# Kernel optimization log

Hardware: AMD Instinct MI355X
Metric: run time of the kernel (lower is better)

The kernel has to match this reference:

```python
import jax, jax.numpy as jnp
import numpy as np

RWKV_K_CLAMP = 60.0
B, T, C = 8, 1024, 1024
LAYER_ID, N_LAYER = 2, 12


def _decay_speed():
    # replicate RWKV_TimeMix.__init__ decay_speed construction
    first = 1
    f1 = 3.0 + (LAYER_ID - first) / (N_LAYER - 1 - first) * (1.2 - 3.0)
    f2 = 0.65 + (LAYER_ID - first) / (N_LAYER - 1 - first) * (0.4 - 0.65)
    if LAYER_ID == first:
        f1 += 0.5
    if LAYER_ID == N_LAYER - 2:
        f2 = 0.4
    if LAYER_ID == N_LAYER - 1:
        f2 = 0.37
    h = np.arange(C, dtype=np.float64)
    return (f2 ** (h / (C - 1) * 7.0)) * f1


def setup_inputs() -> dict:
    key = jax.random.key(0)
    ks = jax.random.split(key, 6)
    scale = 1.0 / np.sqrt(C)
    time_mix = np.ones((C,), np.float32)
    time_mix[: C // 2] = 0.0
    return {
        "x": jax.random.normal(ks[0], (B, T, C), jnp.float32),
        "time_decay": jnp.asarray(np.log(_decay_speed()), jnp.float32),  # (C,)
        "time_first": jnp.full((C,), np.log(0.3), jnp.float32),
        "time_mix": jnp.asarray(time_mix),
        "combined_mix": jnp.full((C,), 0.01, jnp.float32),
        "Wk": jax.random.normal(ks[1], (C, C), jnp.float32) * scale,
        "Wv": jax.random.normal(ks[2], (C, C), jnp.float32) * scale,
        "Wr": jax.random.normal(ks[3], (C, C), jnp.float32) * scale,
        "Wo": jax.random.normal(ks[4], (C, C), jnp.float32) * scale,
    }


def _wkv(w, u, k, v):
    # w,u: (C,); k,v: (B,T,C). Numerically-stable decayed linear recurrence
    # (RWKV wkv kernel: running-max, like online softmax).
    b = k.shape[0]
    init = (
        jnp.zeros((b, C), k.dtype),            # numerator state a
        jnp.zeros((b, C), k.dtype),            # denominator state b
        jnp.full((b, C), -1e38, k.dtype),      # running max exponent p
    )

    def step(carry, kv):
        a, bb, p = carry
        kt, vt = kv  # (B,C)
        no = jnp.maximum(p, u + kt)
        e1 = jnp.exp(p - no)
        e2 = jnp.exp(u + kt - no)
        y = (e1 * a + e2 * vt) / (e1 * bb + e2)
        no2 = jnp.maximum(w + p, kt)
        e1 = jnp.exp(w + p - no2)
        e2 = jnp.exp(kt - no2)
        return (e1 * a + e2 * vt, e1 * bb + e2, no2), y

    _, y = jax.lax.scan(step, init, (k.transpose(1, 0, 2), v.transpose(1, 0, 2)))
    return y.transpose(1, 0, 2)  # (B,T,C)


def reference(x, time_decay, time_first, time_mix, combined_mix, Wk, Wv, Wr, Wo):
    b, t, c = x.shape
    zrow = jnp.zeros((b, 1, c), x.dtype)
    x_m1 = jnp.concatenate([zrow, x[:, :-1, :]], axis=1)   # time_shift / x_{t-1}
    x_p1 = jnp.concatenate([x[:, 1:, :], zrow], axis=1)    # x_{t+1}
    half = c // 2
    x_comb = jnp.concatenate([x_m1[:, :, :half], x_p1[:, :, half:]], axis=-1)
    xm = x * time_mix + x_m1 * (1.0 - time_mix) + x_comb * combined_mix
    k = jnp.exp(jnp.minimum(jnp.einsum("btc,dc->btd", xm, Wk), RWKV_K_CLAMP))
    v = jnp.einsum("btc,dc->btd", xm, Wv)
    r = jnp.einsum("btc,dc->btd", xm, Wr)
    wkv = _wkv(time_decay / t, time_first / t, k, v)
    return jnp.einsum("btc,dc->btd", jax.nn.sigmoid(r) * wkv, Wo)
```

## Files before the change

kernel.cpp:

```cpp
#include <hip/hip_runtime.h>
#include <hip/hip_bf16.h>
#include <stdint.h>

#define B_SZ 8
#define T_LEN 1024
#define C_DIM 1024
#define M_ROWS (B_SZ * T_LEN)
#define NCH 32
#define CHL (T_LEN / NCH)

typedef unsigned short ushort_t;
typedef __attribute__((ext_vector_type(8))) short short8;
typedef __attribute__((ext_vector_type(4))) float f32x4;
typedef __attribute__((ext_vector_type(4))) unsigned short us4;

static __device__ __forceinline__ float bf2f(ushort_t u) {
  union { unsigned int i; float f; } x; x.i = ((unsigned int)u) << 16; return x.f;
}
static __device__ __forceinline__ ushort_t f2bf(float f) {
  union { float f; unsigned int i; } x; x.f = f;
  unsigned int r = x.i + 0x7fffu + ((x.i >> 16) & 1u);
  return (ushort_t)(r >> 16);
}

static __device__ __forceinline__ void gload_lds16(const void* g, void* l) {
  __builtin_amdgcn_global_load_lds(
      (const __attribute__((address_space(1))) void*)g,
      (__attribute__((address_space(3))) void*)l, 16, 0, 0);
}

__global__ void cvt_w_kernel(const float* __restrict__ wk, const float* __restrict__ wv,
                             const float* __restrict__ wr, const float* __restrict__ wo,
                             ushort_t* __restrict__ out) {
  int gid = blockIdx.x * 256 + threadIdx.x;
  int which = gid >> 18;
  int off = (gid << 2) & ((1 << 20) - 1);
  const float* src = which == 0 ? wk : which == 1 ? wv : which == 2 ? wr : wo;
  float4 v = *(const float4*)(src + off);
  us4 o = {f2bf(v.x), f2bf(v.y), f2bf(v.z), f2bf(v.w)};
  *(us4*)(out + (size_t)gid * 4) = o;
}

__global__ void xm_kernel(const float* __restrict__ x, const float* __restrict__ tm,
                          const float* __restrict__ cm, ushort_t* __restrict__ xmb) {
  int gid = blockIdx.x * 256 + threadIdx.x;
  int c4 = (gid & (C_DIM / 4 - 1)) * 4;
  int t = (gid >> 8) & (T_LEN - 1);
  const float4 zero = {0.f, 0.f, 0.f, 0.f};
  float4 xv = *(const float4*)(x + (size_t)gid * 4);
  float4 xp = (t > 0) ? *(const float4*)(x + (size_t)gid * 4 - C_DIM) : zero;
  float4 xn = (t < T_LEN - 1) ? *(const float4*)(x + (size_t)gid * 4 + C_DIM) : zero;
  float4 tmv = *(const float4*)(tm + c4);
  float4 cmv = *(const float4*)(cm + c4);
  float4 xc = (c4 < C_DIM / 2) ? xp : xn;
  us4 o;
  o.x = f2bf(xv.x * tmv.x + xp.x * (1.f - tmv.x) + xc.x * cmv.x);
  o.y = f2bf(xv.y * tmv.y + xp.y * (1.f - tmv.y) + xc.y * cmv.y);
  o.z = f2bf(xv.z * tmv.z + xp.z * (1.f - tmv.z) + xc.z * cmv.z);
  o.w = f2bf(xv.w * tmv.w + xp.w * (1.f - tmv.w) + xc.w * cmv.w);
  *(us4*)(xmb + (size_t)gid * 4) = o;
}

template <int FUSED>
__global__ __launch_bounds__(256) void gemm_bt(const ushort_t* __restrict__ A,
                                               const ushort_t* __restrict__ Bw,
                                               float* __restrict__ outF,
                                               ushort_t* __restrict__ outV,
                                               ushort_t* __restrict__ outR) {
  constexpr int K = 1024;
  constexpr int NT = K / 32;
  __shared__ ushort_t As[2][128 * 32];
  __shared__ ushort_t Bs[2][128 * 32];

  const int tid = threadIdx.x;
  const int lane = tid & 63;
  const int wave = tid >> 6;

  const int bid = blockIdx.x;
  const int xcd = bid & 7;
  const int r = bid >> 3;
  const int bm = (xcd * 8 + (r & 7)) * 128;
  const int jb = r >> 3;
  const int mode = FUSED ? (jb >> 3) : 3;
  const int bn = FUSED ? (jb & 7) * 128 : jb * 128;
  const ushort_t* Bp = FUSED ? (Bw + ((size_t)(jb >> 3) << 20)) : Bw;

  const int wr = (wave >> 1) * 64;
  const int wc = (wave & 1) * 64;

  f32x4 acc[4][4];
#pragma unroll
  for (int m = 0; m < 4; ++m)
#pragma unroll
    for (int n = 0; n < 4; ++n) acc[m][n] = (f32x4){0.f, 0.f, 0.f, 0.f};

  const int srow = tid >> 2;
  const int scol = (((tid & 3) ^ ((srow >> 1) & 3)) * 8);
  const ushort_t* Ag = A + (size_t)(bm + srow) * K + scol;
  const ushort_t* Bg = Bp + (size_t)(bn + srow) * K + scol;
  ushort_t* AsP0 = &As[0][tid * 8];
  ushort_t* BsP0 = &Bs[0][tid * 8];
  ushort_t* AsP1 = &As[1][tid * 8];
  ushort_t* BsP1 = &Bs[1][tid * 8];

  const int fr = lane & 15;
  const int kq = lane >> 4;
  const int ps = (kq ^ ((fr >> 1) & 3)) * 8;

  auto stage = [&](int buf, int k0) {
    ushort_t* ap = buf ? AsP1 : AsP0;
    ushort_t* bp = buf ? BsP1 : BsP0;
    gload_lds16(Ag + k0, ap);
    gload_lds16(Ag + (size_t)64 * K + k0, ap + 64 * 32);
    gload_lds16(Bg + k0, bp);
    gload_lds16(Bg + (size_t)64 * K + k0, bp + 64 * 32);
  };

  stage(0, 0);
  asm volatile("s_waitcnt vmcnt(0)" ::: "memory");
  __syncthreads();

  int cur = 0;
  for (int t = 0; t < NT; ++t) {
    if (t < NT - 1) stage(cur ^ 1, (t + 1) * 32);
    short8 af[4], bfr[4];
#pragma unroll
    for (int m = 0; m < 4; ++m)
      af[m] = *(const short8*)&As[cur][(wr + m * 16 + fr) * 32 + ps];
#pragma unroll
    for (int n = 0; n < 4; ++n)
      bfr[n] = *(const short8*)&Bs[cur][(wc + n * 16 + fr) * 32 + ps];
#pragma unroll
    for (int m = 0; m < 4; ++m)
#pragma unroll
      for (int n = 0; n < 4; ++n)
        acc[m][n] = __builtin_amdgcn_mfma_f32_16x16x32_bf16(af[m], bfr[n], acc[m][n], 0, 0, 0);
    asm volatile("s_waitcnt vmcnt(0)" ::: "memory");
    __syncthreads();
    cur ^= 1;
  }

  const int crow0 = (lane >> 4) * 4;
#pragma unroll
  for (int m = 0; m < 4; ++m)
#pragma unroll
    for (int n = 0; n < 4; ++n)
#pragma unroll
      for (int j = 0; j < 4; ++j) {
        float v = acc[m][n][j];
        size_t idx = (size_t)(bm + wr + m * 16 + crow0 + j) * C_DIM + (bn + wc + n * 16 + fr);
        if (mode == 0) {
          outF[idx] = __expf(fminf(v, 60.f));
        } else if (mode == 1) {
          outV[idx] = f2bf(v);
        } else if (mode == 2) {
          outR[idx] = f2bf(1.f / (1.f + __expf(-v)));
        } else {
          outF[idx] = v;
        }
      }
}

__global__ void wkv_phaseA(const float* __restrict__ kk, const ushort_t* __restrict__ vv,
                           const float* __restrict__ td,
                           float* __restrict__ sa, float* __restrict__ sb,
                           float* __restrict__ sp) {
  int gid = blockIdx.x * 256 + threadIdx.x;
  int c = gid & (C_DIM - 1);
  int ch = (gid >> 10) & (NCH - 1);
  int b = gid >> 15;
  float w = td[c] * (1.f / T_LEN);
  size_t base = ((size_t)b * T_LEN + ch * CHL) * C_DIM + c;
  float a = 0.f, bb = 0.f, p = -1e38f;
  for (int t = 0; t < CHL; ++t) {
    float kt = kk[base + (size_t)t * C_DIM];
    float vt = bf2f(vv[base + (size_t)t * C_DIM]);
    float no2 = fmaxf(w + p, kt);
    float e1 = __expf(w + p - no2);
    float e2 = __expf(kt - no2);
    a = e1 * a + e2 * vt;
    bb = e1 * bb + e2;
    p = no2;
  }
  sa[gid] = a; sb[gid] = bb; sp[gid] = p;
}

__global__ void wkv_phaseC2(const float* __restrict__ kk, const ushort_t* __restrict__ vv,
                            const ushort_t* __restrict__ sr, const float* __restrict__ td,
                            const float* __restrict__ tf,
                            const float* __restrict__ sa, const float* __restrict__ sb,
                            const float* __restrict__ sp, ushort_t* __restrict__ sy) {
  int gid = blockIdx.x * 256 + threadIdx.x;
  int c = gid & (C_DIM - 1);
  int ch = (gid >> 10) & (NCH - 1);
  int b = gid >> 15;
  float w = td[c] * (1.f / T_LEN);
  float u = tf[c] * (1.f / T_LEN);
  float wL = w * (float)CHL;

  float a = 0.f, bb = 0.f, p = -1e38f;
  size_t sbase = ((size_t)b * NCH) * C_DIM + c;
  for (int j = 0; j < ch; ++j) {
    float ac = sa[sbase + (size_t)j * C_DIM];
    float bc = sb[sbase + (size_t)j * C_DIM];
    float pc = sp[sbase + (size_t)j * C_DIM];
    float pn = fmaxf(p + wL, pc);
    float e1 = __expf(p + wL - pn);
    float e2 = __expf(pc - pn);
    a = e1 * a + e2 * ac;
    bb = e1 * bb + e2 * bc;
    p = pn;
  }

  size_t base = ((size_t)b * T_LEN + ch * CHL) * C_DIM + c;
  for (int t = 0; t < CHL; ++t) {
    float kt = kk[base + (size_t)t * C_DIM];
    float vt = bf2f(vv[base + (size_t)t * C_DIM]);
    float no = fmaxf(p, u + kt);
    float e1 = __expf(p - no);
    float e2 = __expf(u + kt - no);
    float y = (e1 * a + e2 * vt) / (e1 * bb + e2);
    float srv = bf2f(sr[base + (size_t)t * C_DIM]);
    sy[base + (size_t)t * C_DIM] = f2bf(srv * y);
    float no2 = fmaxf(w + p, kt);
    e1 = __expf(w + p - no2);
    e2 = __expf(kt - no2);
    a = e1 * a + e2 * vt;
    bb = e1 * bb + e2;
    p = no2;
  }
}

extern "C" void kernel_launch(void* const* d_in, const int* in_sizes, int n_in,
                              void* d_out, int out_size, void* d_ws, size_t ws_size,
                              hipStream_t stream) {
  const float* x  = (const float*)d_in[0];
  const float* td = (const float*)d_in[1];
  const float* tf = (const float*)d_in[2];
  const float* tm = (const float*)d_in[3];
  const float* cm = (const float*)d_in[4];
  const float* Wk = (const float*)d_in[5];
  const float* Wv = (const float*)d_in[6];
  const float* Wr = (const float*)d_in[7];
  const float* Wo = (const float*)d_in[8];

  const size_t MC = (size_t)M_ROWS * C_DIM;
  const size_t CC = (size_t)C_DIM * C_DIM;

  char* ws = (char*)d_ws;
  ushort_t* xmb = (ushort_t*)ws; ws += MC * 2;
  ushort_t* Wb  = (ushort_t*)ws; ws += 4 * CC * 2;
  float*    kk  = (float*)ws;    ws += MC * 4;
  ushort_t* vv  = (ushort_t*)ws; ws += MC * 2;
  ushort_t* sr  = (ushort_t*)ws; ws += MC * 2;
  ushort_t* sy  = (ushort_t*)ws; ws += MC * 2;
  float* sa = (float*)ws; ws += (size_t)B_SZ * NCH * C_DIM * 4;
  float* sb = (float*)ws; ws += (size_t)B_SZ * NCH * C_DIM * 4;
  float* sp = (float*)ws; ws += (size_t)B_SZ * NCH * C_DIM * 4;

  cvt_w_kernel<<<(4 * CC / 4) / 256, 256, 0, stream>>>(Wk, Wv, Wr, Wo, Wb);
  xm_kernel<<<(MC / 4) / 256, 256, 0, stream>>>(x, tm, cm, xmb);

  gemm_bt<1><<<dim3(1536), 256, 0, stream>>>(xmb, Wb, kk, vv, sr);

  wkv_phaseA<<<(B_SZ * NCH * C_DIM) / 256, 256, 0, stream>>>(kk, vv, td, sa, sb, sp);
  wkv_phaseC2<<<(B_SZ * NCH * C_DIM) / 256, 256, 0, stream>>>(kk, vv, sr, td, tf, sa, sb, sp, sy);

  gemm_bt<0><<<dim3(512), 256, 0, stream>>>(sy, Wb + 3 * CC, (float*)d_out, nullptr, nullptr);
}
```

Measured before the change: 166.0 us.

## Enlarge fused QKV GEMM tiles, deepen K-step in output GEMM, store k as bf16

The fused k/v/r GEMM moves to 256x256 tiles with 512 threads and 8 waves, giving 384 blocks. This raises operand reuse per loaded byte. The output projection GEMM gets its own kernel with a 64-wide K step and an 8-way XOR swizzle, which halves the number of barrier iterations. The exp(k) intermediate is now stored as bf16 instead of fp32 to cut memory traffic in the WKV passes, at some precision cost on values that can reach exp(60).

```diff
diff --git a/kernel.cpp b/kernel.cpp
--- a/kernel.cpp
+++ b/kernel.cpp
@@ -61,59 +61,58 @@
   *(us4*)(xmb + (size_t)gid * 4) = o;
 }
 
-template <int FUSED>
-__global__ __launch_bounds__(256) void gemm_bt(const ushort_t* __restrict__ A,
-                                               const ushort_t* __restrict__ Bw,
-                                               float* __restrict__ outF,
-                                               ushort_t* __restrict__ outV,
-                                               ushort_t* __restrict__ outR) {
+__global__ __launch_bounds__(512, 2) void gemm_fused(const ushort_t* __restrict__ A,
+                                                     const ushort_t* __restrict__ Bw,
+                                                     ushort_t* __restrict__ outK,
+                                                     ushort_t* __restrict__ outV,
+                                                     ushort_t* __restrict__ outR) {
   constexpr int K = 1024;
   constexpr int NT = K / 32;
-  __shared__ ushort_t As[2][128 * 32];
-  __shared__ ushort_t Bs[2][128 * 32];
+  __shared__ ushort_t As[2][256 * 32];
+  __shared__ ushort_t Bs[2][256 * 32];
 
   const int tid = threadIdx.x;
-  const int lane = tid & 63;
-  const int wave = tid >> 6;
+  const int l = tid & 63;
+  const int w = tid >> 6;
+  const int wm = w >> 2;
+  const int wn = w & 3;
+  const int fr = l & 15;
+  const int kq = l >> 4;
+  const int ps = (kq ^ ((fr >> 1) & 3)) * 8;
 
   const int bid = blockIdx.x;
   const int xcd = bid & 7;
-  const int r = bid >> 3;
-  const int bm = (xcd * 8 + (r & 7)) * 128;
-  const int jb = r >> 3;
-  const int mode = FUSED ? (jb >> 3) : 3;
-  const int bn = FUSED ? (jb & 7) * 128 : jb * 128;
-  const ushort_t* Bp = FUSED ? (Bw + ((size_t)(jb >> 3) << 20)) : Bw;
-
-  const int wr = (wave >> 1) * 64;
-  const int wc = (wave & 1) * 64;
-
-  f32x4 acc[4][4];
-#pragma unroll
-  for (int m = 0; m < 4; ++m)
+  const int idx = bid >> 3;
+  const int jb = idx >> 2;
+  const int bm = (xcd * 4 + (idx & 3)) * 256;
+  const int mode = jb >> 2;
+  const int bn = (jb & 3) * 256;
+  const ushort_t* Bp = Bw + ((size_t)mode << 20);
+
+  f32x4 acc[8][4];
+#pragma unroll
+  for (int m = 0; m < 8; ++m)
 #pragma unroll
     for (int n = 0; n < 4; ++n) acc[m][n] = (f32x4){0.f, 0.f, 0.f, 0.f};
 
-  const int srow = tid >> 2;
-  const int scol = (((tid & 3) ^ ((srow >> 1) & 3)) * 8);
-  const ushort_t* Ag = A + (size_t)(bm + srow) * K + scol;
-  const ushort_t* Bg = Bp + (size_t)(bn + srow) * K + scol;
-  ushort_t* AsP0 = &As[0][tid * 8];
-  ushort_t* BsP0 = &Bs[0][tid * 8];
-  ushort_t* AsP1 = &As[1][tid * 8];
-  ushort_t* BsP1 = &Bs[1][tid * 8];
-
-  const int fr = lane & 15;
-  const int kq = lane >> 4;
-  const int ps = (kq ^ ((fr >> 1) & 3)) * 8;
+  int srow[2], scol[2];
+#pragma unroll
+  for (int i = 0; i < 2; ++i) {
+    int row = w * 32 + i * 16 + (l >> 2);
+    srow[i] = row;
+    scol[i] = ((l & 3) ^ ((row >> 1) & 3)) * 8;
+  }
+  const ushort_t* AgB = A + (size_t)bm * K;
+  const ushort_t* BgB = Bp + (size_t)bn * K;
+  const int dst0 = w * 1024 + l * 8;
 
   auto stage = [&](int buf, int k0) {
-    ushort_t* ap = buf ? AsP1 : AsP0;
-    ushort_t* bp = buf ? BsP1 : BsP0;
-    gload_lds16(Ag + k0, ap);
-    gload_lds16(Ag + (size_t)64 * K + k0, ap + 64 * 32);
-    gload_lds16(Bg + k0, bp);
-    gload_lds16(Bg + (size_t)64 * K + k0, bp + 64 * 32);
+#pragma unroll
+    for (int i = 0; i < 2; ++i)
+      gload_lds16(AgB + (size_t)srow[i] * K + scol[i] + k0, &As[buf][dst0 + i * 512]);
+#pragma unroll
+    for (int i = 0; i < 2; ++i)
+      gload_lds16(BgB + (size_t)srow[i] * K + scol[i] + k0, &Bs[buf][dst0 + i * 512]);
   };
 
   stage(0, 0);
@@ -123,45 +122,136 @@
   int cur = 0;
   for (int t = 0; t < NT; ++t) {
     if (t < NT - 1) stage(cur ^ 1, (t + 1) * 32);
-    short8 af[4], bfr[4];
-#pragma unroll
-    for (int m = 0; m < 4; ++m)
-      af[m] = *(const short8*)&As[cur][(wr + m * 16 + fr) * 32 + ps];
-#pragma unroll
-    for (int n = 0; n < 4; ++n)
-      bfr[n] = *(const short8*)&Bs[cur][(wc + n * 16 + fr) * 32 + ps];
-#pragma unroll
-    for (int m = 0; m < 4; ++m)
-#pragma unroll
-      for (int n = 0; n < 4; ++n)
-        acc[m][n] = __builtin_amdgcn_mfma_f32_16x16x32_bf16(af[m], bfr[n], acc[m][n], 0, 0, 0);
+    short8 af[8], bfr[4];
+#pragma unroll
+    for (int mf = 0; mf < 8; ++mf)
+      af[mf] = *(const short8*)&As[cur][(wm * 128 + mf * 16 + fr) * 32 + ps];
+#pragma unroll
+    for (int nf = 0; nf < 4; ++nf)
+      bfr[nf] = *(const short8*)&Bs[cur][(wn * 64 + nf * 16 + fr) * 32 + ps];
+#pragma unroll
+    for (int mf = 0; mf < 8; ++mf)
+#pragma unroll
+      for (int nf = 0; nf < 4; ++nf)
+        acc[mf][nf] = __builtin_amdgcn_mfma_f32_16x16x32_bf16(af[mf], bfr[nf], acc[mf][nf], 0, 0, 0);
     asm volatile("s_waitcnt vmcnt(0)" ::: "memory");
     __syncthreads();
     cur ^= 1;
   }
 
-  const int crow0 = (lane >> 4) * 4;
-#pragma unroll
-  for (int m = 0; m < 4; ++m)
-#pragma unroll
-    for (int n = 0; n < 4; ++n)
+#pragma unroll
+  for (int mf = 0; mf < 8; ++mf)
+#pragma unroll
+    for (int nf = 0; nf < 4; ++nf)
 #pragma unroll
       for (int j = 0; j < 4; ++j) {
-        float v = acc[m][n][j];
-        size_t idx = (size_t)(bm + wr + m * 16 + crow0 + j) * C_DIM + (bn + wc + n * 16 + fr);
+        float v = acc[mf][nf][j];
+        size_t ridx = (size_t)(bm + wm * 128 + mf * 16 + kq * 4 + j) * C_DIM +
+                      (bn + wn * 64 + nf * 16 + fr);
         if (mode == 0) {
-          outF[idx] = __expf(fminf(v, 60.f));
+          outK[ridx] = f2bf(__expf(fminf(v, 60.f)));
         } else if (mode == 1) {
-          outV[idx] = f2bf(v);
-        } else if (mode == 2) {
-          outR[idx] = f2bf(1.f / (1.f + __expf(-v)));
+          outV[ridx] = f2bf(v);
         } else {
-          outF[idx] = v;
+          outR[ridx] = f2bf(1.f / (1.f + __expf(-v)));
         }
       }
 }
 
-__global__ void wkv_phaseA(const float* __restrict__ kk, const ushort_t* __restrict__ vv,
+__global__ __launch_bounds__(256, 2) void gemm_out(const ushort_t* __restrict__ A,
+                                                   const ushort_t* __restrict__ Bw,
+                                                   float* __restrict__ outF) {
+  constexpr int K = 1024;
+  constexpr int NT = K / 64;
+  __shared__ ushort_t As[2][128 * 64];
+  __shared__ ushort_t Bs[2][128 * 64];
+
+  const int tid = threadIdx.x;
+  const int l = tid & 63;
+  const int wave = tid >> 6;
+  const int fr = l & 15;
+  const int kq = l >> 4;
+
+  const int bid = blockIdx.x;
+  const int xcd = bid & 7;
+  const int idx = bid >> 3;
+  const int jb = idx >> 3;
+  const int bm = (xcd * 8 + (idx & 7)) * 128;
+  const int bn = jb * 128;
+
+  const int wr = (wave >> 1) * 64;
+  const int wc = (wave & 1) * 64;
+
+  f32x4 acc[4][4];
+#pragma unroll
+  for (int m = 0; m < 4; ++m)
+#pragma unroll
+    for (int n = 0; n < 4; ++n) acc[m][n] = (f32x4){0.f, 0.f, 0.f, 0.f};
+
+  int srow[4], scol[4];
+#pragma unroll
+  for (int j = 0; j < 4; ++j) {
+    int row = wave * 32 + j * 8 + (l >> 3);
+    srow[j] = row;
+    scol[j] = ((l & 7) ^ (row & 7)) * 8;
+  }
+  const ushort_t* AgB = A + (size_t)bm * K;
+  const ushort_t* BgB = Bw + (size_t)bn * K;
+  const int dst0 = wave * 2048 + l * 8;
+
+  auto stage = [&](int buf, int k0) {
+#pragma unroll
+    for (int j = 0; j < 4; ++j)
+      gload_lds16(AgB + (size_t)srow[j] * K + scol[j] + k0, &As[buf][dst0 + j * 512]);
+#pragma unroll
+    for (int j = 0; j < 4; ++j)
+      gload_lds16(BgB + (size_t)srow[j] * K + scol[j] + k0, &Bs[buf][dst0 + j * 512]);
+  };
+
+  stage(0, 0);
+  asm volatile("s_waitcnt vmcnt(0)" ::: "memory");
+  __syncthreads();
+
+  const int ps0 = ((0 * 4 + kq) ^ (fr & 7)) * 8;
+  const int ps1 = ((1 * 4 + kq) ^ (fr & 7)) * 8;
+
+  int cur = 0;
+  for (int t = 0; t < NT; ++t) {
+    if (t < NT - 1) stage(cur ^ 1, (t + 1) * 64);
+    short8 af[4][2], bfr[4][2];
+#pragma unroll
+    for (int m = 0; m < 4; ++m) {
+      af[m][0] = *(const short8*)&As[cur][(wr + m * 16 + fr) * 64 + ps0];
+      af[m][1] = *(const short8*)&As[cur][(wr + m * 16 + fr) * 64 + ps1];
+    }
+#pragma unroll
+    for (int n = 0; n < 4; ++n) {
+      bfr[n][0] = *(const short8*)&Bs[cur][(wc + n * 16 + fr) * 64 + ps0];
+      bfr[n][1] = *(const short8*)&Bs[cur][(wc + n * 16 + fr) * 64 + ps1];
+    }
+#pragma unroll
+    for (int m = 0; m < 4; ++m)
+#pragma unroll
+      for (int n = 0; n < 4; ++n)
+#pragma unroll
+        for (int ks = 0; ks < 2; ++ks)
+          acc[m][n] = __builtin_amdgcn_mfma_f32_16x16x32_bf16(af[m][ks], bfr[n][ks], acc[m][n], 0, 0, 0);
+    asm volatile("s_waitcnt vmcnt(0)" ::: "memory");
+    __syncthreads();
+    cur ^= 1;
+  }
+
+#pragma unroll
+  for (int m = 0; m < 4; ++m)
+#pragma unroll
+    for (int n = 0; n < 4; ++n)
+#pragma unroll
+      for (int j = 0; j < 4; ++j)
+        outF[(size_t)(bm + wr + m * 16 + kq * 4 + j) * C_DIM + (bn + wc + n * 16 + fr)] =
+            acc[m][n][j];
+}
+
+__global__ void wkv_phaseA(const ushort_t* __restrict__ kk, const ushort_t* __restrict__ vv,
                            const float* __restrict__ td,
                            float* __restrict__ sa, float* __restrict__ sb,
                            float* __restrict__ sp) {
@@ -173,7 +263,7 @@
   size_t base = ((size_t)b * T_LEN + ch * CHL) * C_DIM + c;
   float a = 0.f, bb = 0.f, p = -1e38f;
   for (int t = 0; t < CHL; ++t) {
-    float kt = kk[base + (size_t)t * C_DIM];
+    float kt = bf2f(kk[base + (size_t)t * C_DIM]);
     float vt = bf2f(vv[base + (size_t)t * C_DIM]);
     float no2 = fmaxf(w + p, kt);
     float e1 = __expf(w + p - no2);
@@ -185,7 +275,7 @@
   sa[gid] = a; sb[gid] = bb; sp[gid] = p;
 }
 
-__global__ void wkv_phaseC2(const float* __restrict__ kk, const ushort_t* __restrict__ vv,
+__global__ void wkv_phaseC2(const ushort_t* __restrict__ kk, const ushort_t* __restrict__ vv,
                             const ushort_t* __restrict__ sr, const float* __restrict__ td,
                             const float* __restrict__ tf,
                             const float* __restrict__ sa, const float* __restrict__ sb,
@@ -214,7 +304,7 @@
 
   size_t base = ((size_t)b * T_LEN + ch * CHL) * C_DIM + c;
   for (int t = 0; t < CHL; ++t) {
-    float kt = kk[base + (size_t)t * C_DIM];
+    float kt = bf2f(kk[base + (size_t)t * C_DIM]);
     float vt = bf2f(vv[base + (size_t)t * C_DIM]);
     float no = fmaxf(p, u + kt);
     float e1 = __expf(p - no);
@@ -250,7 +340,7 @@
   char* ws = (char*)d_ws;
   ushort_t* xmb = (ushort_t*)ws; ws += MC * 2;
   ushort_t* Wb  = (ushort_t*)ws; ws += 4 * CC * 2;
-  float*    kk  = (float*)ws;    ws += MC * 4;
+  ushort_t* kk  = (ushort_t*)ws; ws += MC * 2;
   ushort_t* vv  = (ushort_t*)ws; ws += MC * 2;
   ushort_t* sr  = (ushort_t*)ws; ws += MC * 2;
   ushort_t* sy  = (ushort_t*)ws; ws += MC * 2;
@@ -261,10 +351,10 @@
   cvt_w_kernel<<<(4 * CC / 4) / 256, 256, 0, stream>>>(Wk, Wv, Wr, Wo, Wb);
   xm_kernel<<<(MC / 4) / 256, 256, 0, stream>>>(x, tm, cm, xmb);
 
-  gemm_bt<1><<<dim3(1536), 256, 0, stream>>>(xmb, Wb, kk, vv, sr);
+  gemm_fused<<<dim3(384), 512, 0, stream>>>(xmb, Wb, kk, vv, sr);
 
   wkv_phaseA<<<(B_SZ * NCH * C_DIM) / 256, 256, 0, stream>>>(kk, vv, td, sa, sb, sp);
   wkv_phaseC2<<<(B_SZ * NCH * C_DIM) / 256, 256, 0, stream>>>(kk, vv, sr, td, tf, sa, sb, sp, sy);
 
-  gemm_bt<0><<<dim3(512), 256, 0, stream>>>(sy, Wb + 3 * CC, (float*)d_out, nullptr, nullptr);
-}
+  gemm_out<<<dim3(512), 256, 0, stream>>>(sy, Wb + 3 * CC, (float*)d_out);
+}
```

Result: slower. 185.1 us (+11.5%).

## Triple-buffer GEMM LDS pipeline and store k activations as bf16

Applied to the files above, without the earlier changes.

The GEMM moves from double to triple buffering of LDS tiles. Two stages stay in flight, waiting with vmcnt(4) and a raw s_barrier instead of draining all loads every k-step, and the launch bounds are raised to 3 blocks per CU. Separately, exp(k) is stored as bf16 instead of fp32, which halves that tensor's write and read traffic in the GEMM epilogue and both wkv passes. In exchange, LDS use per block grows and k loses precision, and k can be very large before the clamp at exp(60).

```diff
diff --git a/kernel.cpp b/kernel.cpp
--- a/kernel.cpp
+++ b/kernel.cpp
@@ -62,15 +62,16 @@
 }
 
 template <int FUSED>
-__global__ __launch_bounds__(256) void gemm_bt(const ushort_t* __restrict__ A,
-                                               const ushort_t* __restrict__ Bw,
-                                               float* __restrict__ outF,
-                                               ushort_t* __restrict__ outV,
-                                               ushort_t* __restrict__ outR) {
+__global__ __launch_bounds__(256, 3) void gemm_pipe(const ushort_t* __restrict__ A,
+                                                    const ushort_t* __restrict__ Bw,
+                                                    float* __restrict__ outF,
+                                                    ushort_t* __restrict__ outK,
+                                                    ushort_t* __restrict__ outV,
+                                                    ushort_t* __restrict__ outR) {
   constexpr int K = 1024;
   constexpr int NT = K / 32;
-  __shared__ ushort_t As[2][128 * 32];
-  __shared__ ushort_t Bs[2][128 * 32];
+  __shared__ ushort_t As[3][128 * 32];
+  __shared__ ushort_t Bs[3][128 * 32];
 
   const int tid = threadIdx.x;
   const int lane = tid & 63;
@@ -98,49 +99,63 @@
   const int scol = (((tid & 3) ^ ((srow >> 1) & 3)) * 8);
   const ushort_t* Ag = A + (size_t)(bm + srow) * K + scol;
   const ushort_t* Bg = Bp + (size_t)(bn + srow) * K + scol;
-  ushort_t* AsP0 = &As[0][tid * 8];
-  ushort_t* BsP0 = &Bs[0][tid * 8];
-  ushort_t* AsP1 = &As[1][tid * 8];
-  ushort_t* BsP1 = &Bs[1][tid * 8];
 
   const int fr = lane & 15;
   const int kq = lane >> 4;
   const int ps = (kq ^ ((fr >> 1) & 3)) * 8;
 
-  auto stage = [&](int buf, int k0) {
-    ushort_t* ap = buf ? AsP1 : AsP0;
-    ushort_t* bp = buf ? BsP1 : BsP0;
+  auto stage = [&](int buf, int kt) {
+    const int k0 = kt * 32;
+    ushort_t* ap = &As[buf][tid * 8];
+    ushort_t* bp = &Bs[buf][tid * 8];
     gload_lds16(Ag + k0, ap);
     gload_lds16(Ag + (size_t)64 * K + k0, ap + 64 * 32);
     gload_lds16(Bg + k0, bp);
     gload_lds16(Bg + (size_t)64 * K + k0, bp + 64 * 32);
   };
 
+#define MFMA_STEP(BUF)                                                        \
+  {                                                                           \
+    short8 af[4], bfr[4];                                                     \
+    _Pragma("unroll") for (int m = 0; m < 4; ++m)                             \
+        af[m] = *(const short8*)&As[BUF][(wr + m * 16 + fr) * 32 + ps];       \
+    _Pragma("unroll") for (int n = 0; n < 4; ++n)                             \
+        bfr[n] = *(const short8*)&Bs[BUF][(wc + n * 16 + fr) * 32 + ps];      \
+    _Pragma("unroll") for (int m = 0; m < 4; ++m)                             \
+        _Pragma("unroll") for (int n = 0; n < 4; ++n)                         \
+            acc[m][n] = __builtin_amdgcn_mfma_f32_16x16x32_bf16(              \
+                af[m], bfr[n], acc[m][n], 0, 0, 0);                           \
+  }
+
+#define VMW4 asm volatile("s_waitcnt vmcnt(4)" ::: "memory")
+#define VMW0 asm volatile("s_waitcnt vmcnt(0)" ::: "memory")
+
   stage(0, 0);
-  asm volatile("s_waitcnt vmcnt(0)" ::: "memory");
-  __syncthreads();
-
-  int cur = 0;
-  for (int t = 0; t < NT; ++t) {
-    if (t < NT - 1) stage(cur ^ 1, (t + 1) * 32);
-    short8 af[4], bfr[4];
-#pragma unroll
-    for (int m = 0; m < 4; ++m)
-      af[m] = *(const short8*)&As[cur][(wr + m * 16 + fr) * 32 + ps];
-#pragma unroll
-    for (int n = 0; n < 4; ++n)
-      bfr[n] = *(const short8*)&Bs[cur][(wc + n * 16 + fr) * 32 + ps];
-#pragma unroll
-    for (int m = 0; m < 4; ++m)
-#pragma unroll
-      for (int n = 0; n < 4; ++n)
-        acc[m][n] = __builtin_amdgcn_mfma_f32_16x16x32_bf16(af[m], bfr[n], acc[m][n], 0, 0, 0);
-    asm volatile("s_waitcnt vmcnt(0)" ::: "memory");
-    __syncthreads();
-    cur ^= 1;
-  }
-
-  const int crow0 = (lane >> 4) * 4;
+  stage(1, 1);
+  VMW4;
+  __builtin_amdgcn_s_barrier();
+
+#pragma unroll 1
+  for (int i = 0; i < 10; ++i) {
+    const int t0 = 3 * i;
+    stage(2, t0 + 2);
+    MFMA_STEP(0);
+    VMW4;
+    __builtin_amdgcn_s_barrier();
+    stage(0, t0 + 3);
+    MFMA_STEP(1);
+    VMW4;
+    __builtin_amdgcn_s_barrier();
+    stage(1, t0 + 4);
+    MFMA_STEP(2);
+    VMW4;
+    __builtin_amdgcn_s_barrier();
+  }
+  MFMA_STEP(0);
+  VMW0;
+  __builtin_amdgcn_s_barrier();
+  MFMA_STEP(1);
+
 #pragma unroll
   for (int m = 0; m < 4; ++m)
 #pragma unroll
@@ -148,9 +163,9 @@
 #pragma unroll
       for (int j = 0; j < 4; ++j) {
         float v = acc[m][n][j];
-        size_t idx = (size_t)(bm + wr + m * 16 + crow0 + j) * C_DIM + (bn + wc + n * 16 + fr);
+        size_t idx = (size_t)(bm + wr + m * 16 + kq * 4 + j) * C_DIM + (bn + wc + n * 16 + fr);
         if (mode == 0) {
-          outF[idx] = __expf(fminf(v, 60.f));
+          outK[idx] = f2bf(__expf(fminf(v, 60.f)));
         } else if (mode == 1) {
           outV[idx] = f2bf(v);
         } else if (mode == 2) {
@@ -159,9 +174,12 @@
           outF[idx] = v;
         }
       }
-}
-
-__global__ void wkv_phaseA(const float* __restrict__ kk, const ushort_t* __restrict__ vv,
+#undef MFMA_STEP
+#undef VMW4
+#undef VMW0
+}
+
+__global__ void wkv_phaseA(const ushort_t* __restrict__ kk, const ushort_t* __restrict__ vv,
                            const float* __restrict__ td,
                            float* __restrict__ sa, float* __restrict__ sb,
                            float* __restrict__ sp) {
@@ -173,7 +191,7 @@
   size_t base = ((size_t)b * T_LEN + ch * CHL) * C_DIM + c;
   float a = 0.f, bb = 0.f, p = -1e38f;
   for (int t = 0; t < CHL; ++t) {
-    float kt = kk[base + (size_t)t * C_DIM];
+    float kt = bf2f(kk[base + (size_t)t * C_DIM]);
     float vt = bf2f(vv[base + (size_t)t * C_DIM]);
     float no2 = fmaxf(w + p, kt);
     float e1 = __expf(w + p - no2);
@@ -185,7 +203,7 @@
   sa[gid] = a; sb[gid] = bb; sp[gid] = p;
 }
 
-__global__ void wkv_phaseC2(const float* __restrict__ kk, const ushort_t* __restrict__ vv,
+__global__ void wkv_phaseC2(const ushort_t* __restrict__ kk, const ushort_t* __restrict__ vv,
                             const ushort_t* __restrict__ sr, const float* __restrict__ td,
                             const float* __restrict__ tf,
                             const float* __restrict__ sa, const float* __restrict__ sb,
@@ -214,7 +232,7 @@
 
   size_t base = ((size_t)b * T_LEN + ch * CHL) * C_DIM + c;
   for (int t = 0; t < CHL; ++t) {
-    float kt = kk[base + (size_t)t * C_DIM];
+    float kt = bf2f(kk[base + (size_t)t * C_DIM]);
     float vt = bf2f(vv[base + (size_t)t * C_DIM]);
     float no = fmaxf(p, u + kt);
     float e1 = __expf(p - no);
@@ -250,7 +268,7 @@
   char* ws = (char*)d_ws;
   ushort_t* xmb = (ushort_t*)ws; ws += MC * 2;
   ushort_t* Wb  = (ushort_t*)ws; ws += 4 * CC * 2;
-  float*    kk  = (float*)ws;    ws += MC * 4;
+  ushort_t* kk  = (ushort_t*)ws; ws += MC * 2;
   ushort_t* vv  = (ushort_t*)ws; ws += MC * 2;
   ushort_t* sr  = (ushort_t*)ws; ws += MC * 2;
   ushort_t* sy  = (ushort_t*)ws; ws += MC * 2;
@@ -261,10 +279,10 @@
   cvt_w_kernel<<<(4 * CC / 4) / 256, 256, 0, stream>>>(Wk, Wv, Wr, Wo, Wb);
   xm_kernel<<<(MC / 4) / 256, 256, 0, stream>>>(x, tm, cm, xmb);
 
-  gemm_bt<1><<<dim3(1536), 256, 0, stream>>>(xmb, Wb, kk, vv, sr);
+  gemm_pipe<1><<<dim3(1536), 256, 0, stream>>>(xmb, Wb, nullptr, kk, vv, sr);
 
   wkv_phaseA<<<(B_SZ * NCH * C_DIM) / 256, 256, 0, stream>>>(kk, vv, td, sa, sb, sp);
   wkv_phaseC2<<<(B_SZ * NCH * C_DIM) / 256, 256, 0, stream>>>(kk, vv, sr, td, tf, sa, sb, sp, sy);
 
-  gemm_bt<0><<<dim3(512), 256, 0, stream>>>(sy, Wb + 3 * CC, (float*)d_out, nullptr, nullptr);
-}
+  gemm_pipe<0><<<dim3(512), 256, 0, stream>>>(sy, Wb + 3 * CC, (float*)d_out, nullptr, nullptr, nullptr);
+}
```

Result: faster. 158.0 us (-4.8%).
